# Performance work log

Hardware: AMD Instinct MI355X
Metric: run time of the kernel (lower is better)

The kernel has to match this reference:

```python
import jax, jax.numpy as jnp
import numpy as np

# Swin block config (matches init_kwargs)
NUM_HEADS = 6
WS = 7          # window_size
SHIFT = 3       # shift_size
C = 192         # channels; keras MHA key_dim = channels
KEY_DIM = C


def setup_inputs() -> dict:
    key = jax.random.key(0)
    ks = jax.random.split(key, 9)
    B, H, W = 16, 112, 112
    s = 0.02
    x = jax.random.normal(ks[0], (B, H, W, C), dtype=jnp.float32)
    # keras MultiHeadAttention params: Wq/Wk/Wv [C, heads, key_dim], Wo [heads, key_dim, C]
    Wq = jax.random.normal(ks[1], (C, NUM_HEADS, KEY_DIM), dtype=jnp.float32) * s
    bq = jnp.zeros((NUM_HEADS, KEY_DIM), dtype=jnp.float32)
    Wk = jax.random.normal(ks[2], (C, NUM_HEADS, KEY_DIM), dtype=jnp.float32) * s
    bk = jnp.zeros((NUM_HEADS, KEY_DIM), dtype=jnp.float32)
    Wv = jax.random.normal(ks[3], (C, NUM_HEADS, KEY_DIM), dtype=jnp.float32) * s
    bv = jnp.zeros((NUM_HEADS, KEY_DIM), dtype=jnp.float32)
    Wo = jax.random.normal(ks[4], (NUM_HEADS, KEY_DIM, C), dtype=jnp.float32) * s
    bo = jnp.zeros((C,), dtype=jnp.float32)
    return {"x": x, "Wq": Wq, "bq": bq, "Wk": Wk, "bk": bk,
            "Wv": Wv, "bv": bv, "Wo": Wo, "bo": bo}


def reference(x, Wq, bq, Wk, bk, Wv, bv, Wo, bo):
    B, H, W, _ = x.shape
    # shifted window: roll up-left
    x = jnp.roll(x, shift=(-SHIFT, -SHIFT), axis=(1, 2))
    # window partition (== tf.image.extract_patches + reshape):
    # [B,H,W,C] -> [B*nW, ws*ws, C] with row-major window-token order
    nH, nW = H // WS, W // WS
    win = x.reshape(B, nH, WS, nW, WS, C).transpose(0, 1, 3, 2, 4, 5)
    win = win.reshape(B * nH * nW, WS * WS, C)
    q = jnp.einsum('btc,chd->bthd', win, Wq) + bq
    k = jnp.einsum('btc,chd->bthd', win, Wk) + bk
    v = jnp.einsum('btc,chd->bthd', win, Wv) + bv
    scale = 1.0 / jnp.sqrt(jnp.asarray(KEY_DIM, dtype=q.dtype))
    scores = jnp.einsum('bthd,bshd->bhts', q, k) * scale  # [nWin, heads, 49, 49]
    attn = jax.nn.softmax(scores, axis=-1)
    o = jnp.einsum('bhts,bshd->bthd', attn, v)
    o = jnp.einsum('bthd,hdc->btc', o, Wo) + bo
    # NOTE: original code merges windows with a PLAIN reshape (does not invert
    # the partition); replicate exactly for faithfulness.
    out = o.reshape(B, H, W, C)
    out = jnp.roll(out, shift=(SHIFT, SHIFT), axis=(1, 2))
    return out
```

## Files before the change

kernel.cpp:

```cpp
#include <hip/hip_runtime.h>
#include <hip/hip_bf16.h>

typedef __bf16 bf16_t;
typedef __bf16 bf16x4 __attribute__((ext_vector_type(4)));
typedef __bf16 bf16x8 __attribute__((ext_vector_type(8)));
typedef float  f32x4  __attribute__((ext_vector_type(4)));

#define NH    6
#define CH    192
#define HW    112
#define SHIFT 3

#define XLD 200
#define ULD 72

#define X_OFF   0
#define T_OFF   (64 * XLD)
#define P_OFF   T_OFF
#define VOT_OFF (T_OFF + 64 * ULD)
#define LDS_ELEMS (VOT_OFF + 192 * ULD)
#define LDS_BYTES (LDS_ELEMS * 2)

#define U_OFF_ELEMS  (NH * CH * CH)
#define BU_OFF_BYTES (2 * NH * CH * CH * 2)
#define W1_OFF_BYTES (BU_OFF_BYTES + NH * CH * 4)

__global__ void prep_gt(const float* __restrict__ Wq, const float* __restrict__ Wk,
                        bf16_t* __restrict__ gt) {
  __shared__ float wk_row[CH];
  int h = blockIdx.x / CH, cp = blockIdx.x % CH;
  int c = threadIdx.x;
  wk_row[c] = Wk[(cp * NH + h) * CH + c];
  __syncthreads();
  float acc = 0.f;
  for (int d = 0; d < CH; ++d)
    acc += wk_row[d] * Wq[(c * NH + h) * CH + d];
  int tile = cp >> 4, l15 = cp & 15;
  int ks = c >> 5, lg = (c >> 3) & 3, e = c & 7;
  gt[((((h * 12 + tile) * 6 + ks) << 6) + lg * 16 + l15) * 8 + e] = (bf16_t)acc;
}

__global__ void prep_u(const float* __restrict__ Wv, const float* __restrict__ Wo,
                       bf16_t* __restrict__ u_out) {
  __shared__ float wv_row[CH];
  int h = blockIdx.x / CH, ci = blockIdx.x % CH;
  int t = threadIdx.x;
  wv_row[t] = Wv[(ci * NH + h) * CH + t];
  __syncthreads();
  float acc = 0.f;
  for (int d = 0; d < CH; ++d)
    acc += wv_row[d] * Wo[(h * CH + d) * CH + t];
  int tile = t >> 4, l15 = t & 15;
  int ks = ci >> 5, lg = (ci >> 3) & 3, e = ci & 7;
  u_out[((((h * 12 + tile) * 6 + ks) << 6) + lg * 16 + l15) * 8 + e] = (bf16_t)acc;
}

__global__ void prep_bu(const float* __restrict__ bv, const float* __restrict__ Wo,
                        float* __restrict__ bu) {
  int h = blockIdx.x, c = threadIdx.x;
  float acc = 0.f;
  for (int d = 0; d < CH; ++d)
    acc += bv[h * CH + d] * Wo[(h * CH + d) * CH + c];
  bu[h * CH + c] = acc;
}

__global__ void prep_w1(const float* __restrict__ Wk, const float* __restrict__ bq,
                        float* __restrict__ w1) {
  int h = blockIdx.x, cp = threadIdx.x;
  float acc = 0.f;
  for (int d = 0; d < CH; ++d)
    acc += Wk[(cp * NH + h) * CH + d] * bq[h * CH + d];
  w1[h * CH + cp] = acc;
}

__global__ __launch_bounds__(256, 2) void swin_fused(
    const float* __restrict__ x,
    const float* __restrict__ bo,
    const bf16_t* __restrict__ wts,
    const float* __restrict__ bu, const float* __restrict__ w1,
    float* __restrict__ out) {
  extern __shared__ char smem_raw[];
  bf16_t* lds  = (bf16_t*)smem_raw;
  bf16_t* Xl   = lds + X_OFF;
  bf16_t* Tl   = lds + T_OFF;
  bf16_t* Pl   = lds + P_OFF;
  bf16_t* VOtl = lds + VOT_OFF;

  const int tid  = threadIdx.x;
  const int wave = tid >> 6;
  const int lane = tid & 63;
  const int l15  = lane & 15;
  const int lg   = lane >> 4;

  const int blk = blockIdx.x;
  const int b   = blk >> 8;
  const int rem = blk & 255;
  const int wi  = rem >> 4, wj = rem & 15;

  for (int idx = tid; idx < 15 * 100; idx += 256) {
    int row = 49 + idx / 100, c2 = (idx % 100) * 2;
    *(unsigned int*)&Xl[row * XLD + c2] = 0u;
  }
  for (int idx = tid; idx < 49 * 48; idx += 256) {
    int t = idx / 48, q4 = idx % 48;
    int hs = wi * 7 + t / 7 + SHIFT; if (hs >= HW) hs -= HW;
    int ws2 = wj * 7 + t % 7 + SHIFT; if (ws2 >= HW) ws2 -= HW;
    const float4 v = *(const float4*)&x[(((b * HW + hs) * HW) + ws2) * CH + q4 * 4];
    bf16x4 pk = { (bf16_t)v.x, (bf16_t)v.y, (bf16_t)v.z, (bf16_t)v.w };
    *(bf16x4*)&Xl[t * XLD + q4 * 4] = pk;
  }

  const int wm = wave * 3;
  const float scale = 0.07216878364870322f;
  f32x4 yacc[3][4] = {};

  for (int h = 0; h < NH; ++h) {
    __syncthreads();
    {
      const bf16_t* gt = wts;
      f32x4 acc[3][4] = {};
#pragma unroll
      for (int ks = 0; ks < 6; ++ks) {
        bf16x8 af[3], bfr[4];
#pragma unroll
        for (int mi = 0; mi < 3; ++mi)
          af[mi] = *(const bf16x8*)&gt[((((h * 12 + wm + mi) * 6 + ks) << 6) + lane) * 8];
#pragma unroll
        for (int ni = 0; ni < 4; ++ni)
          bfr[ni] = *(const bf16x8*)&Xl[(ni * 16 + l15) * XLD + ks * 32 + lg * 8];
#pragma unroll
        for (int mi = 0; mi < 3; ++mi)
#pragma unroll
          for (int ni = 0; ni < 4; ++ni)
            acc[mi][ni] = __builtin_amdgcn_mfma_f32_16x16x32_bf16(af[mi], bfr[ni], acc[mi][ni], 0, 0, 0);
      }
      const float* w1h = w1 + h * CH;
#pragma unroll
      for (int mi = 0; mi < 3; ++mi) {
        int cp0 = (wm + mi) * 16 + lg * 4;
        const f32x4 ww = *(const f32x4*)&w1h[cp0];
#pragma unroll
        for (int ni = 0; ni < 4; ++ni) {
          int i = ni * 16 + l15;
          if (i < 49) {
            bf16x4 pk = { (bf16_t)(acc[mi][ni][0] + ww[0]), (bf16_t)(acc[mi][ni][1] + ww[1]),
                          (bf16_t)(acc[mi][ni][2] + ww[2]), (bf16_t)(acc[mi][ni][3] + ww[3]) };
            *(bf16x4*)&Tl[i * XLD + cp0] = pk;
          }
        }
      }
    }
    __syncthreads();
    bf16x4 psave[4];
    f32x4 vacc[3][4] = {};
    const bf16_t* U_w = wts + U_OFF_ELEMS;
    {
      f32x4 sacc[4] = {};
#pragma unroll
      for (int ks = 0; ks < 6; ++ks) {
        bf16x8 af[4], bfu[3];
#pragma unroll
        for (int mi = 0; mi < 4; ++mi)
          af[mi] = *(const bf16x8*)&Xl[(mi * 16 + l15) * XLD + ks * 32 + lg * 8];
        bf16x8 bt = *(const bf16x8*)&Tl[(wave * 16 + l15) * XLD + ks * 32 + lg * 8];
#pragma unroll
        for (int mi = 0; mi < 3; ++mi)
          bfu[mi] = *(const bf16x8*)&U_w[((((h * 12 + wm + mi) * 6 + ks) << 6) + lane) * 8];
#pragma unroll
        for (int mj = 0; mj < 4; ++mj)
          sacc[mj] = __builtin_amdgcn_mfma_f32_16x16x32_bf16(af[mj], bt, sacc[mj], 0, 0, 0);
#pragma unroll
        for (int mi = 0; mi < 3; ++mi)
#pragma unroll
          for (int ms = 0; ms < 4; ++ms)
            vacc[mi][ms] = __builtin_amdgcn_mfma_f32_16x16x32_bf16(af[ms], bfu[mi], vacc[mi][ms], 0, 0, 0);
      }
      float mx = -1e30f;
#pragma unroll
      for (int mj = 0; mj < 4; ++mj)
#pragma unroll
        for (int r = 0; r < 4; ++r) {
          int j = mj * 16 + lg * 4 + r;
          if (j < 49) mx = fmaxf(mx, sacc[mj][r]);
        }
      mx = fmaxf(mx, __shfl_xor(mx, 16));
      mx = fmaxf(mx, __shfl_xor(mx, 32));
      float p[4][4];
      float sum = 0.f;
#pragma unroll
      for (int mj = 0; mj < 4; ++mj)
#pragma unroll
        for (int r = 0; r < 4; ++r) {
          int j = mj * 16 + lg * 4 + r;
          float e = (j < 49) ? __expf((sacc[mj][r] - mx) * scale) : 0.f;
          p[mj][r] = e;
          sum += e;
        }
      sum += __shfl_xor(sum, 16);
      sum += __shfl_xor(sum, 32);
      float inv = 1.f / sum;
#pragma unroll
      for (int mj = 0; mj < 4; ++mj) {
        bf16x4 pk = { (bf16_t)(p[mj][0] * inv), (bf16_t)(p[mj][1] * inv),
                      (bf16_t)(p[mj][2] * inv), (bf16_t)(p[mj][3] * inv) };
        psave[mj] = pk;
      }
    }
    __syncthreads();
    {
      const float* bu_h = bu + h * CH;
      int i = wave * 16 + l15;
#pragma unroll
      for (int mj = 0; mj < 4; ++mj)
        *(bf16x4*)&Pl[i * ULD + mj * 16 + lg * 4] = psave[mj];
#pragma unroll
      for (int mi = 0; mi < 3; ++mi) {
        int c = (wm + mi) * 16 + l15;
        float bb = bu_h[c];
#pragma unroll
        for (int ms = 0; ms < 4; ++ms) {
          int s0 = ms * 16 + lg * 4;
          bf16x4 pk = { (bf16_t)(vacc[mi][ms][0] + bb), (bf16_t)(vacc[mi][ms][1] + bb),
                        (bf16_t)(vacc[mi][ms][2] + bb), (bf16_t)(vacc[mi][ms][3] + bb) };
          *(bf16x4*)&VOtl[c * ULD + s0] = pk;
        }
      }
    }
    __syncthreads();
    {
#pragma unroll
      for (int ks = 0; ks < 2; ++ks) {
        bf16x8 af[3], bfr[4];
#pragma unroll
        for (int mi = 0; mi < 3; ++mi)
          af[mi] = *(const bf16x8*)&VOtl[((wm + mi) * 16 + l15) * ULD + ks * 32 + lg * 8];
#pragma unroll
        for (int ni = 0; ni < 4; ++ni)
          bfr[ni] = *(const bf16x8*)&Pl[(ni * 16 + l15) * ULD + ks * 32 + lg * 8];
#pragma unroll
        for (int mi = 0; mi < 3; ++mi)
#pragma unroll
          for (int ni = 0; ni < 4; ++ni)
            yacc[mi][ni] = __builtin_amdgcn_mfma_f32_16x16x32_bf16(af[mi], bfr[ni], yacc[mi][ni], 0, 0, 0);
      }
    }
  }

#pragma unroll
  for (int ni = 0; ni < 4; ++ni) {
    int t = ni * 16 + l15;
    if (t < 49) {
      int pos = rem * 49 + t;
      int hp = pos / 112, wp = pos % 112;
      hp += SHIFT; if (hp >= HW) hp -= HW;
      wp += SHIFT; if (wp >= HW) wp -= HW;
      float* op = out + (((b * HW + hp) * HW) + wp) * CH;
#pragma unroll
      for (int mi = 0; mi < 3; ++mi) {
        int c0 = (wm + mi) * 16 + lg * 4;
        f32x4 v = yacc[mi][ni];
        v[0] += bo[c0]; v[1] += bo[c0 + 1]; v[2] += bo[c0 + 2]; v[3] += bo[c0 + 3];
        *(f32x4*)&op[c0] = v;
      }
    }
  }
}

extern "C" void kernel_launch(void* const* d_in, const int* in_sizes, int n_in,
                              void* d_out, int out_size, void* d_ws, size_t ws_size,
                              hipStream_t stream) {
  const float* x  = (const float*)d_in[0];
  const float* Wq = (const float*)d_in[1];
  const float* bq = (const float*)d_in[2];
  const float* Wk = (const float*)d_in[3];
  const float* Wv = (const float*)d_in[5];
  const float* bv = (const float*)d_in[6];
  const float* Wo = (const float*)d_in[7];
  const float* bo = (const float*)d_in[8];
  float* out = (float*)d_out;
  bf16_t* wts = (bf16_t*)d_ws;
  float*  bu  = (float*)((char*)d_ws + BU_OFF_BYTES);
  float*  w1  = (float*)((char*)d_ws + W1_OFF_BYTES);

  prep_gt<<<NH * CH, CH, 0, stream>>>(Wq, Wk, wts);
  prep_u<<<NH * CH, CH, 0, stream>>>(Wv, Wo, wts + U_OFF_ELEMS);
  prep_bu<<<NH, CH, 0, stream>>>(bv, Wo, bu);
  prep_w1<<<NH, CH, 0, stream>>>(Wk, bq, w1);

  (void)hipFuncSetAttribute((const void*)swin_fused,
                            hipFuncAttributeMaxDynamicSharedMemorySize, LDS_BYTES);
  swin_fused<<<dim3(4096), dim3(256), LDS_BYTES, stream>>>(x, bo, wts, bu, w1, out);
}
```

Measured before the change: 473.3 us.

## Restructure per-head MFMA loops to cut registers and drop P staging in LDS

Splits the T and VO projections into smaller accumulator chunks and moves the VO computation after softmax, so fewer live accumulators are needed and launch bounds can rise to three blocks per CU. The softmax probabilities stay in registers as MFMA B operands instead of being written to LDS, which removes the P buffer and shrinks the LDS footprint. The output accumulation is re-mapped so each wave owns 16 tokens across all 192 channels. The trade-offs are less operand reuse per LDS/global load, extra unpacking shuffles, and possible register spilling under the tighter bound.

```diff
diff --git a/kernel.cpp b/kernel.cpp
--- a/kernel.cpp
+++ b/kernel.cpp
@@ -16,9 +16,8 @@
 
 #define X_OFF   0
 #define T_OFF   (64 * XLD)
-#define P_OFF   T_OFF
-#define VOT_OFF (T_OFF + 64 * ULD)
-#define LDS_ELEMS (VOT_OFF + 192 * ULD)
+#define VOT_OFF T_OFF
+#define LDS_ELEMS (T_OFF + 192 * ULD)
 #define LDS_BYTES (LDS_ELEMS * 2)
 
 #define U_OFF_ELEMS  (NH * CH * CH)
@@ -73,7 +72,7 @@
   w1[h * CH + cp] = acc;
 }
 
-__global__ __launch_bounds__(256, 2) void swin_fused(
+__global__ __launch_bounds__(256, 3) void swin_fused(
     const float* __restrict__ x,
     const float* __restrict__ bo,
     const bf16_t* __restrict__ wts,
@@ -83,7 +82,6 @@
   bf16_t* lds  = (bf16_t*)smem_raw;
   bf16_t* Xl   = lds + X_OFF;
   bf16_t* Tl   = lds + T_OFF;
-  bf16_t* Pl   = lds + P_OFF;
   bf16_t* VOtl = lds + VOT_OFF;
 
   const int tid  = threadIdx.x;
@@ -112,68 +110,50 @@
 
   const int wm = wave * 3;
   const float scale = 0.07216878364870322f;
-  f32x4 yacc[3][4] = {};
+  f32x4 yacc[12] = {};
 
   for (int h = 0; h < NH; ++h) {
     __syncthreads();
     {
       const bf16_t* gt = wts;
-      f32x4 acc[3][4] = {};
+      const float* w1h = w1 + h * CH;
+#pragma unroll
+      for (int ni = 0; ni < 4; ++ni) {
+        f32x4 acc[3] = {};
+#pragma unroll
+        for (int ks = 0; ks < 6; ++ks) {
+          bf16x8 bfr = *(const bf16x8*)&Xl[(ni * 16 + l15) * XLD + ks * 32 + lg * 8];
+#pragma unroll
+          for (int mi = 0; mi < 3; ++mi) {
+            bf16x8 af = *(const bf16x8*)&gt[((((h * 12 + wm + mi) * 6 + ks) << 6) + lane) * 8];
+            acc[mi] = __builtin_amdgcn_mfma_f32_16x16x32_bf16(af, bfr, acc[mi], 0, 0, 0);
+          }
+        }
+        int i = ni * 16 + l15;
+        if (i < 49) {
+#pragma unroll
+          for (int mi = 0; mi < 3; ++mi) {
+            int cp0 = (wm + mi) * 16 + lg * 4;
+            const f32x4 ww = *(const f32x4*)&w1h[cp0];
+            bf16x4 pk = { (bf16_t)(acc[mi][0] + ww[0]), (bf16_t)(acc[mi][1] + ww[1]),
+                          (bf16_t)(acc[mi][2] + ww[2]), (bf16_t)(acc[mi][3] + ww[3]) };
+            *(bf16x4*)&Tl[i * XLD + cp0] = pk;
+          }
+        }
+      }
+    }
+    __syncthreads();
+    bf16x4 psave[4];
+    {
+      f32x4 sacc[4] = {};
 #pragma unroll
       for (int ks = 0; ks < 6; ++ks) {
-        bf16x8 af[3], bfr[4];
-#pragma unroll
-        for (int mi = 0; mi < 3; ++mi)
-          af[mi] = *(const bf16x8*)&gt[((((h * 12 + wm + mi) * 6 + ks) << 6) + lane) * 8];
-#pragma unroll
-        for (int ni = 0; ni < 4; ++ni)
-          bfr[ni] = *(const bf16x8*)&Xl[(ni * 16 + l15) * XLD + ks * 32 + lg * 8];
-#pragma unroll
-        for (int mi = 0; mi < 3; ++mi)
-#pragma unroll
-          for (int ni = 0; ni < 4; ++ni)
-            acc[mi][ni] = __builtin_amdgcn_mfma_f32_16x16x32_bf16(af[mi], bfr[ni], acc[mi][ni], 0, 0, 0);
-      }
-      const float* w1h = w1 + h * CH;
-#pragma unroll
-      for (int mi = 0; mi < 3; ++mi) {
-        int cp0 = (wm + mi) * 16 + lg * 4;
-        const f32x4 ww = *(const f32x4*)&w1h[cp0];
-#pragma unroll
-        for (int ni = 0; ni < 4; ++ni) {
-          int i = ni * 16 + l15;
-          if (i < 49) {
-            bf16x4 pk = { (bf16_t)(acc[mi][ni][0] + ww[0]), (bf16_t)(acc[mi][ni][1] + ww[1]),
-                          (bf16_t)(acc[mi][ni][2] + ww[2]), (bf16_t)(acc[mi][ni][3] + ww[3]) };
-            *(bf16x4*)&Tl[i * XLD + cp0] = pk;
-          }
-        }
-      }
-    }
-    __syncthreads();
-    bf16x4 psave[4];
-    f32x4 vacc[3][4] = {};
-    const bf16_t* U_w = wts + U_OFF_ELEMS;
-    {
-      f32x4 sacc[4] = {};
-#pragma unroll
-      for (int ks = 0; ks < 6; ++ks) {
-        bf16x8 af[4], bfu[3];
-#pragma unroll
-        for (int mi = 0; mi < 4; ++mi)
-          af[mi] = *(const bf16x8*)&Xl[(mi * 16 + l15) * XLD + ks * 32 + lg * 8];
         bf16x8 bt = *(const bf16x8*)&Tl[(wave * 16 + l15) * XLD + ks * 32 + lg * 8];
 #pragma unroll
-        for (int mi = 0; mi < 3; ++mi)
-          bfu[mi] = *(const bf16x8*)&U_w[((((h * 12 + wm + mi) * 6 + ks) << 6) + lane) * 8];
-#pragma unroll
-        for (int mj = 0; mj < 4; ++mj)
-          sacc[mj] = __builtin_amdgcn_mfma_f32_16x16x32_bf16(af[mj], bt, sacc[mj], 0, 0, 0);
-#pragma unroll
-        for (int mi = 0; mi < 3; ++mi)
-#pragma unroll
-          for (int ms = 0; ms < 4; ++ms)
-            vacc[mi][ms] = __builtin_amdgcn_mfma_f32_16x16x32_bf16(af[ms], bfu[mi], vacc[mi][ms], 0, 0, 0);
+        for (int mj = 0; mj < 4; ++mj) {
+          bf16x8 af = *(const bf16x8*)&Xl[(mj * 16 + l15) * XLD + ks * 32 + lg * 8];
+          sacc[mj] = __builtin_amdgcn_mfma_f32_16x16x32_bf16(af, bt, sacc[mj], 0, 0, 0);
+        }
       }
       float mx = -1e30f;
 #pragma unroll
@@ -208,47 +188,55 @@
     }
     __syncthreads();
     {
+      const bf16_t* U_w = wts + U_OFF_ELEMS;
       const float* bu_h = bu + h * CH;
-      int i = wave * 16 + l15;
-#pragma unroll
-      for (int mj = 0; mj < 4; ++mj)
-        *(bf16x4*)&Pl[i * ULD + mj * 16 + lg * 4] = psave[mj];
 #pragma unroll
       for (int mi = 0; mi < 3; ++mi) {
         int c = (wm + mi) * 16 + l15;
         float bb = bu_h[c];
 #pragma unroll
-        for (int ms = 0; ms < 4; ++ms) {
-          int s0 = ms * 16 + lg * 4;
-          bf16x4 pk = { (bf16_t)(vacc[mi][ms][0] + bb), (bf16_t)(vacc[mi][ms][1] + bb),
-                        (bf16_t)(vacc[mi][ms][2] + bb), (bf16_t)(vacc[mi][ms][3] + bb) };
-          *(bf16x4*)&VOtl[c * ULD + s0] = pk;
-        }
-      }
-    }
-    __syncthreads();
-    {
-#pragma unroll
-      for (int ks = 0; ks < 2; ++ks) {
-        bf16x8 af[3], bfr[4];
-#pragma unroll
-        for (int mi = 0; mi < 3; ++mi)
-          af[mi] = *(const bf16x8*)&VOtl[((wm + mi) * 16 + l15) * ULD + ks * 32 + lg * 8];
-#pragma unroll
-        for (int ni = 0; ni < 4; ++ni)
-          bfr[ni] = *(const bf16x8*)&Pl[(ni * 16 + l15) * ULD + ks * 32 + lg * 8];
-#pragma unroll
-        for (int mi = 0; mi < 3; ++mi)
-#pragma unroll
-          for (int ni = 0; ni < 4; ++ni)
-            yacc[mi][ni] = __builtin_amdgcn_mfma_f32_16x16x32_bf16(af[mi], bfr[ni], yacc[mi][ni], 0, 0, 0);
-      }
-    }
-  }
-
-#pragma unroll
-  for (int ni = 0; ni < 4; ++ni) {
-    int t = ni * 16 + l15;
+        for (int sh = 0; sh < 2; ++sh) {
+          f32x4 vacc[2] = {};
+#pragma unroll
+          for (int ks = 0; ks < 6; ++ks) {
+            bf16x8 bfu = *(const bf16x8*)&U_w[((((h * 12 + wm + mi) * 6 + ks) << 6) + lane) * 8];
+#pragma unroll
+            for (int m2 = 0; m2 < 2; ++m2) {
+              bf16x8 af = *(const bf16x8*)&Xl[((sh * 2 + m2) * 16 + l15) * XLD + ks * 32 + lg * 8];
+              vacc[m2] = __builtin_amdgcn_mfma_f32_16x16x32_bf16(af, bfu, vacc[m2], 0, 0, 0);
+            }
+          }
+#pragma unroll
+          for (int m2 = 0; m2 < 2; ++m2) {
+            int s0 = (sh * 2 + m2) * 16 + lg * 4;
+            bf16x4 pk = { (bf16_t)(vacc[m2][0] + bb), (bf16_t)(vacc[m2][1] + bb),
+                          (bf16_t)(vacc[m2][2] + bb), (bf16_t)(vacc[m2][3] + bb) };
+            *(bf16x4*)&VOtl[c * ULD + s0] = pk;
+          }
+        }
+      }
+    }
+    __syncthreads();
+    {
+      bf16x8 bq8[2];
+      bq8[0] = __builtin_shufflevector(psave[0], psave[1], 0, 1, 2, 3, 4, 5, 6, 7);
+      bq8[1] = __builtin_shufflevector(psave[2], psave[3], 0, 1, 2, 3, 4, 5, 6, 7);
+#pragma unroll
+      for (int mc = 0; mc < 12; ++mc) {
+#pragma unroll
+        for (int kp = 0; kp < 2; ++kp) {
+          const bf16_t* vr = &VOtl[(mc * 16 + l15) * ULD + kp * 32 + lg * 4];
+          bf16x4 a0 = *(const bf16x4*)vr;
+          bf16x4 a1 = *(const bf16x4*)(vr + 16);
+          bf16x8 av = __builtin_shufflevector(a0, a1, 0, 1, 2, 3, 4, 5, 6, 7);
+          yacc[mc] = __builtin_amdgcn_mfma_f32_16x16x32_bf16(av, bq8[kp], yacc[mc], 0, 0, 0);
+        }
+      }
+    }
+  }
+
+  {
+    int t = wave * 16 + l15;
     if (t < 49) {
       int pos = rem * 49 + t;
       int hp = pos / 112, wp = pos % 112;
@@ -256,9 +244,9 @@
       wp += SHIFT; if (wp >= HW) wp -= HW;
       float* op = out + (((b * HW + hp) * HW) + wp) * CH;
 #pragma unroll
-      for (int mi = 0; mi < 3; ++mi) {
-        int c0 = (wm + mi) * 16 + lg * 4;
-        f32x4 v = yacc[mi][ni];
+      for (int mc = 0; mc < 12; ++mc) {
+        int c0 = mc * 16 + lg * 4;
+        f32x4 v = yacc[mc];
         v[0] += bo[c0]; v[1] += bo[c0 + 1]; v[2] += bo[c0 + 2]; v[3] += bo[c0 + 3];
         *(f32x4*)&op[c0] = v;
       }
```

Result: slower. 861.0 us (+81.9%).

## Keep softmax probabilities in registers and defer the PV product to the next head

Applied to the files above, without the earlier changes.

Each wave now keeps its own query rows' softmax probabilities in registers as MFMA B-operands instead of writing them to a shared P buffer. The P·V product is remapped so each wave accumulates all 192 output channels for its 16 tokens. That product is software-pipelined one head behind, running alongside the next head's score computation. This removes the P LDS round trip and one barrier per head, and the V projection is moved after the softmax. In exchange it adds register pressure (12 accumulators plus carried P fragments) and split LDS reads of V.

```diff
diff --git a/kernel.cpp b/kernel.cpp
--- a/kernel.cpp
+++ b/kernel.cpp
@@ -16,8 +16,7 @@
 
 #define X_OFF   0
 #define T_OFF   (64 * XLD)
-#define P_OFF   T_OFF
-#define VOT_OFF (T_OFF + 64 * ULD)
+#define VOT_OFF (2 * 64 * XLD)
 #define LDS_ELEMS (VOT_OFF + 192 * ULD)
 #define LDS_BYTES (LDS_ELEMS * 2)
 
@@ -83,7 +82,6 @@
   bf16_t* lds  = (bf16_t*)smem_raw;
   bf16_t* Xl   = lds + X_OFF;
   bf16_t* Tl   = lds + T_OFF;
-  bf16_t* Pl   = lds + P_OFF;
   bf16_t* VOtl = lds + VOT_OFF;
 
   const int tid  = threadIdx.x;
@@ -109,13 +107,14 @@
     bf16x4 pk = { (bf16_t)v.x, (bf16_t)v.y, (bf16_t)v.z, (bf16_t)v.w };
     *(bf16x4*)&Xl[t * XLD + q4 * 4] = pk;
   }
+  __syncthreads();
 
   const int wm = wave * 3;
   const float scale = 0.07216878364870322f;
-  f32x4 yacc[3][4] = {};
+  f32x4 yacc[12] = {};
+  bf16x8 pq_prev0 = {}, pq_prev1 = {};
 
   for (int h = 0; h < NH; ++h) {
-    __syncthreads();
     {
       const bf16_t* gt = wts;
       f32x4 acc[3][4] = {};
@@ -151,29 +150,35 @@
       }
     }
     __syncthreads();
-    bf16x4 psave[4];
-    f32x4 vacc[3][4] = {};
-    const bf16_t* U_w = wts + U_OFF_ELEMS;
     {
       f32x4 sacc[4] = {};
 #pragma unroll
       for (int ks = 0; ks < 6; ++ks) {
-        bf16x8 af[4], bfu[3];
-#pragma unroll
-        for (int mi = 0; mi < 4; ++mi)
-          af[mi] = *(const bf16x8*)&Xl[(mi * 16 + l15) * XLD + ks * 32 + lg * 8];
         bf16x8 bt = *(const bf16x8*)&Tl[(wave * 16 + l15) * XLD + ks * 32 + lg * 8];
 #pragma unroll
-        for (int mi = 0; mi < 3; ++mi)
-          bfu[mi] = *(const bf16x8*)&U_w[((((h * 12 + wm + mi) * 6 + ks) << 6) + lane) * 8];
-#pragma unroll
-        for (int mj = 0; mj < 4; ++mj)
-          sacc[mj] = __builtin_amdgcn_mfma_f32_16x16x32_bf16(af[mj], bt, sacc[mj], 0, 0, 0);
-#pragma unroll
-        for (int mi = 0; mi < 3; ++mi)
-#pragma unroll
-          for (int ms = 0; ms < 4; ++ms)
-            vacc[mi][ms] = __builtin_amdgcn_mfma_f32_16x16x32_bf16(af[ms], bfu[mi], vacc[mi][ms], 0, 0, 0);
+        for (int mj = 0; mj < 4; ++mj) {
+          bf16x8 af = *(const bf16x8*)&Xl[(mj * 16 + l15) * XLD + ks * 32 + lg * 8];
+          sacc[mj] = __builtin_amdgcn_mfma_f32_16x16x32_bf16(af, bt, sacc[mj], 0, 0, 0);
+        }
+      }
+      if (h > 0) {
+#pragma unroll
+        for (int mc = 0; mc < 12; ++mc) {
+          {
+            const bf16_t* vr = &VOtl[(mc * 16 + l15) * ULD + 0 * 32 + lg * 4];
+            bf16x4 a0 = *(const bf16x4*)vr;
+            bf16x4 a1 = *(const bf16x4*)(vr + 16);
+            bf16x8 av = __builtin_shufflevector(a0, a1, 0, 1, 2, 3, 4, 5, 6, 7);
+            yacc[mc] = __builtin_amdgcn_mfma_f32_16x16x32_bf16(av, pq_prev0, yacc[mc], 0, 0, 0);
+          }
+          {
+            const bf16_t* vr = &VOtl[(mc * 16 + l15) * ULD + 1 * 32 + lg * 4];
+            bf16x4 a0 = *(const bf16x4*)vr;
+            bf16x4 a1 = *(const bf16x4*)(vr + 16);
+            bf16x8 av = __builtin_shufflevector(a0, a1, 0, 1, 2, 3, 4, 5, 6, 7);
+            yacc[mc] = __builtin_amdgcn_mfma_f32_16x16x32_bf16(av, pq_prev1, yacc[mc], 0, 0, 0);
+          }
+        }
       }
       float mx = -1e30f;
 #pragma unroll
@@ -199,20 +204,37 @@
       sum += __shfl_xor(sum, 16);
       sum += __shfl_xor(sum, 32);
       float inv = 1.f / sum;
-#pragma unroll
-      for (int mj = 0; mj < 4; ++mj) {
-        bf16x4 pk = { (bf16_t)(p[mj][0] * inv), (bf16_t)(p[mj][1] * inv),
-                      (bf16_t)(p[mj][2] * inv), (bf16_t)(p[mj][3] * inv) };
-        psave[mj] = pk;
-      }
+      bf16x4 ps0 = { (bf16_t)(p[0][0] * inv), (bf16_t)(p[0][1] * inv),
+                     (bf16_t)(p[0][2] * inv), (bf16_t)(p[0][3] * inv) };
+      bf16x4 ps1 = { (bf16_t)(p[1][0] * inv), (bf16_t)(p[1][1] * inv),
+                     (bf16_t)(p[1][2] * inv), (bf16_t)(p[1][3] * inv) };
+      bf16x4 ps2 = { (bf16_t)(p[2][0] * inv), (bf16_t)(p[2][1] * inv),
+                     (bf16_t)(p[2][2] * inv), (bf16_t)(p[2][3] * inv) };
+      bf16x4 ps3 = { (bf16_t)(p[3][0] * inv), (bf16_t)(p[3][1] * inv),
+                     (bf16_t)(p[3][2] * inv), (bf16_t)(p[3][3] * inv) };
+      pq_prev0 = __builtin_shufflevector(ps0, ps1, 0, 1, 2, 3, 4, 5, 6, 7);
+      pq_prev1 = __builtin_shufflevector(ps2, ps3, 0, 1, 2, 3, 4, 5, 6, 7);
     }
     __syncthreads();
     {
+      const bf16_t* U_w = wts + U_OFF_ELEMS;
       const float* bu_h = bu + h * CH;
-      int i = wave * 16 + l15;
-#pragma unroll
-      for (int mj = 0; mj < 4; ++mj)
-        *(bf16x4*)&Pl[i * ULD + mj * 16 + lg * 4] = psave[mj];
+      f32x4 vacc[3][4] = {};
+#pragma unroll
+      for (int ks = 0; ks < 6; ++ks) {
+        bf16x8 bfu[3], af[4];
+#pragma unroll
+        for (int mi = 0; mi < 3; ++mi)
+          bfu[mi] = *(const bf16x8*)&U_w[((((h * 12 + wm + mi) * 6 + ks) << 6) + lane) * 8];
+#pragma unroll
+        for (int ms = 0; ms < 4; ++ms)
+          af[ms] = *(const bf16x8*)&Xl[(ms * 16 + l15) * XLD + ks * 32 + lg * 8];
+#pragma unroll
+        for (int mi = 0; mi < 3; ++mi)
+#pragma unroll
+          for (int ms = 0; ms < 4; ++ms)
+            vacc[mi][ms] = __builtin_amdgcn_mfma_f32_16x16x32_bf16(af[ms], bfu[mi], vacc[mi][ms], 0, 0, 0);
+      }
 #pragma unroll
       for (int mi = 0; mi < 3; ++mi) {
         int c = (wm + mi) * 16 + l15;
@@ -227,28 +249,30 @@
       }
     }
     __syncthreads();
-    {
-#pragma unroll
-      for (int ks = 0; ks < 2; ++ks) {
-        bf16x8 af[3], bfr[4];
-#pragma unroll
-        for (int mi = 0; mi < 3; ++mi)
-          af[mi] = *(const bf16x8*)&VOtl[((wm + mi) * 16 + l15) * ULD + ks * 32 + lg * 8];
-#pragma unroll
-        for (int ni = 0; ni < 4; ++ni)
-          bfr[ni] = *(const bf16x8*)&Pl[(ni * 16 + l15) * ULD + ks * 32 + lg * 8];
-#pragma unroll
-        for (int mi = 0; mi < 3; ++mi)
-#pragma unroll
-          for (int ni = 0; ni < 4; ++ni)
-            yacc[mi][ni] = __builtin_amdgcn_mfma_f32_16x16x32_bf16(af[mi], bfr[ni], yacc[mi][ni], 0, 0, 0);
-      }
-    }
-  }
-
-#pragma unroll
-  for (int ni = 0; ni < 4; ++ni) {
-    int t = ni * 16 + l15;
+  }
+
+  {
+#pragma unroll
+    for (int mc = 0; mc < 12; ++mc) {
+      {
+        const bf16_t* vr = &VOtl[(mc * 16 + l15) * ULD + 0 * 32 + lg * 4];
+        bf16x4 a0 = *(const bf16x4*)vr;
+        bf16x4 a1 = *(const bf16x4*)(vr + 16);
+        bf16x8 av = __builtin_shufflevector(a0, a1, 0, 1, 2, 3, 4, 5, 6, 7);
+        yacc[mc] = __builtin_amdgcn_mfma_f32_16x16x32_bf16(av, pq_prev0, yacc[mc], 0, 0, 0);
+      }
+      {
+        const bf16_t* vr = &VOtl[(mc * 16 + l15) * ULD + 1 * 32 + lg * 4];
+        bf16x4 a0 = *(const bf16x4*)vr;
+        bf16x4 a1 = *(const bf16x4*)(vr + 16);
+        bf16x8 av = __builtin_shufflevector(a0, a1, 0, 1, 2, 3, 4, 5, 6, 7);
+        yacc[mc] = __builtin_amdgcn_mfma_f32_16x16x32_bf16(av, pq_prev1, yacc[mc], 0, 0, 0);
+      }
+    }
+  }
+
+  {
+    int t = wave * 16 + l15;
     if (t < 49) {
       int pos = rem * 49 + t;
       int hp = pos / 112, wp = pos % 112;
@@ -256,9 +280,9 @@
       wp += SHIFT; if (wp >= HW) wp -= HW;
       float* op = out + (((b * HW + hp) * HW) + wp) * CH;
 #pragma unroll
-      for (int mi = 0; mi < 3; ++mi) {
-        int c0 = (wm + mi) * 16 + lg * 4;
-        f32x4 v = yacc[mi][ni];
+      for (int mc = 0; mc < 12; ++mc) {
+        int c0 = mc * 16 + lg * 4;
+        f32x4 v = yacc[mc];
         v[0] += bo[c0]; v[1] += bo[c0 + 1]; v[2] += bo[c0 + 2]; v[3] += bo[c0 + 3];
         *(f32x4*)&op[c0] = v;
       }
```

Measured after the change: 475.5 us. About the same (+0.5%).

## Double-buffer T/P across heads and keep V·Wo fragments in registers

Applied to the files above, without the earlier changes.

Restructures the per-head loop. The T projection for head h+1 is computed into an alternate LDS buffer while head h's P is consumed, which cuts barriers per head from four to one. The VU product is now produced directly in the MFMA operand layout and kept in registers instead of being staged through LDS, and the output GEMM swaps operand roles, which changes the final store pattern to scalar per-lane writes. Risks are higher register pressure, padding rows of X left uninitialized (their results are masked only partly), and less coalesced output stores.

```diff
diff --git a/kernel.cpp b/kernel.cpp
--- a/kernel.cpp
+++ b/kernel.cpp
@@ -12,13 +12,14 @@
 #define SHIFT 3
 
 #define XLD 200
-#define ULD 72
+#define PLD 68
 
 #define X_OFF   0
-#define T_OFF   (64 * XLD)
-#define P_OFF   T_OFF
-#define VOT_OFF (T_OFF + 64 * ULD)
-#define LDS_ELEMS (VOT_OFF + 192 * ULD)
+#define T0_OFF  9800
+#define T1_OFF  19600
+#define P0_OFF  29400
+#define P1_OFF  33752
+#define LDS_ELEMS 38104
 #define LDS_BYTES (LDS_ELEMS * 2)
 
 #define U_OFF_ELEMS  (NH * CH * CH)
@@ -73,6 +74,52 @@
   w1[h * CH + cp] = acc;
 }
 
+__device__ __forceinline__ void t_phase(const bf16_t* __restrict__ gt,
+                                        const float* __restrict__ w1h,
+                                        const bf16_t* Xl, bf16_t* Tdst,
+                                        int hh, int wm, int lane, int l15, int lg) {
+  f32x4 ww[3];
+#pragma unroll
+  for (int mi = 0; mi < 3; ++mi)
+    ww[mi] = *(const f32x4*)&w1h[(wm + mi) * 16 + lg * 4];
+#pragma unroll
+  for (int ip = 0; ip < 2; ++ip) {
+    f32x4 acc[3][2];
+#pragma unroll
+    for (int mi = 0; mi < 3; ++mi)
+#pragma unroll
+      for (int n2 = 0; n2 < 2; ++n2) acc[mi][n2] = ww[mi];
+#pragma unroll
+    for (int ks = 0; ks < 6; ++ks) {
+      bf16x8 af[3], bfr[2];
+#pragma unroll
+      for (int mi = 0; mi < 3; ++mi)
+        af[mi] = *(const bf16x8*)&gt[((((hh * 12 + wm + mi) * 6 + ks) << 6) + lane) * 8];
+#pragma unroll
+      for (int n2 = 0; n2 < 2; ++n2)
+        bfr[n2] = *(const bf16x8*)&Xl[((ip * 2 + n2) * 16 + l15) * XLD + ks * 32 + lg * 8];
+#pragma unroll
+      for (int mi = 0; mi < 3; ++mi)
+#pragma unroll
+        for (int n2 = 0; n2 < 2; ++n2)
+          acc[mi][n2] = __builtin_amdgcn_mfma_f32_16x16x32_bf16(af[mi], bfr[n2], acc[mi][n2], 0, 0, 0);
+    }
+#pragma unroll
+    for (int mi = 0; mi < 3; ++mi) {
+      int cp0 = (wm + mi) * 16 + lg * 4;
+#pragma unroll
+      for (int n2 = 0; n2 < 2; ++n2) {
+        int i = (ip * 2 + n2) * 16 + l15;
+        if (i < 49) {
+          bf16x4 pk = { (bf16_t)acc[mi][n2][0], (bf16_t)acc[mi][n2][1],
+                        (bf16_t)acc[mi][n2][2], (bf16_t)acc[mi][n2][3] };
+          *(bf16x4*)&Tdst[i * XLD + cp0] = pk;
+        }
+      }
+    }
+  }
+}
+
 __global__ __launch_bounds__(256, 2) void swin_fused(
     const float* __restrict__ x,
     const float* __restrict__ bo,
@@ -80,11 +127,8 @@
     const float* __restrict__ bu, const float* __restrict__ w1,
     float* __restrict__ out) {
   extern __shared__ char smem_raw[];
-  bf16_t* lds  = (bf16_t*)smem_raw;
-  bf16_t* Xl   = lds + X_OFF;
-  bf16_t* Tl   = lds + T_OFF;
-  bf16_t* Pl   = lds + P_OFF;
-  bf16_t* VOtl = lds + VOT_OFF;
+  bf16_t* lds = (bf16_t*)smem_raw;
+  bf16_t* Xl  = lds + X_OFF;
 
   const int tid  = threadIdx.x;
   const int wave = tid >> 6;
@@ -97,10 +141,6 @@
   const int rem = blk & 255;
   const int wi  = rem >> 4, wj = rem & 15;
 
-  for (int idx = tid; idx < 15 * 100; idx += 256) {
-    int row = 49 + idx / 100, c2 = (idx % 100) * 2;
-    *(unsigned int*)&Xl[row * XLD + c2] = 0u;
-  }
   for (int idx = tid; idx < 49 * 48; idx += 256) {
     int t = idx / 48, q4 = idx % 48;
     int hs = wi * 7 + t / 7 + SHIFT; if (hs >= HW) hs -= HW;
@@ -109,71 +149,31 @@
     bf16x4 pk = { (bf16_t)v.x, (bf16_t)v.y, (bf16_t)v.z, (bf16_t)v.w };
     *(bf16x4*)&Xl[t * XLD + q4 * 4] = pk;
   }
+  __syncthreads();
 
   const int wm = wave * 3;
   const float scale = 0.07216878364870322f;
+
+  t_phase(wts, w1, Xl, lds + T0_OFF, 0, wm, lane, l15, lg);
+  __syncthreads();
+
   f32x4 yacc[3][4] = {};
 
   for (int h = 0; h < NH; ++h) {
-    __syncthreads();
-    {
-      const bf16_t* gt = wts;
-      f32x4 acc[3][4] = {};
-#pragma unroll
-      for (int ks = 0; ks < 6; ++ks) {
-        bf16x8 af[3], bfr[4];
-#pragma unroll
-        for (int mi = 0; mi < 3; ++mi)
-          af[mi] = *(const bf16x8*)&gt[((((h * 12 + wm + mi) * 6 + ks) << 6) + lane) * 8];
-#pragma unroll
-        for (int ni = 0; ni < 4; ++ni)
-          bfr[ni] = *(const bf16x8*)&Xl[(ni * 16 + l15) * XLD + ks * 32 + lg * 8];
-#pragma unroll
-        for (int mi = 0; mi < 3; ++mi)
-#pragma unroll
-          for (int ni = 0; ni < 4; ++ni)
-            acc[mi][ni] = __builtin_amdgcn_mfma_f32_16x16x32_bf16(af[mi], bfr[ni], acc[mi][ni], 0, 0, 0);
-      }
-      const float* w1h = w1 + h * CH;
-#pragma unroll
-      for (int mi = 0; mi < 3; ++mi) {
-        int cp0 = (wm + mi) * 16 + lg * 4;
-        const f32x4 ww = *(const f32x4*)&w1h[cp0];
-#pragma unroll
-        for (int ni = 0; ni < 4; ++ni) {
-          int i = ni * 16 + l15;
-          if (i < 49) {
-            bf16x4 pk = { (bf16_t)(acc[mi][ni][0] + ww[0]), (bf16_t)(acc[mi][ni][1] + ww[1]),
-                          (bf16_t)(acc[mi][ni][2] + ww[2]), (bf16_t)(acc[mi][ni][3] + ww[3]) };
-            *(bf16x4*)&Tl[i * XLD + cp0] = pk;
-          }
-        }
-      }
-    }
-    __syncthreads();
+    const bf16_t* Tcur = lds + ((h & 1) ? T1_OFF : T0_OFF);
+    bf16_t*       Pcur = lds + ((h & 1) ? P1_OFF : P0_OFF);
+
     bf16x4 psave[4];
-    f32x4 vacc[3][4] = {};
-    const bf16_t* U_w = wts + U_OFF_ELEMS;
     {
       f32x4 sacc[4] = {};
 #pragma unroll
       for (int ks = 0; ks < 6; ++ks) {
-        bf16x8 af[4], bfu[3];
-#pragma unroll
-        for (int mi = 0; mi < 4; ++mi)
-          af[mi] = *(const bf16x8*)&Xl[(mi * 16 + l15) * XLD + ks * 32 + lg * 8];
-        bf16x8 bt = *(const bf16x8*)&Tl[(wave * 16 + l15) * XLD + ks * 32 + lg * 8];
-#pragma unroll
-        for (int mi = 0; mi < 3; ++mi)
-          bfu[mi] = *(const bf16x8*)&U_w[((((h * 12 + wm + mi) * 6 + ks) << 6) + lane) * 8];
-#pragma unroll
-        for (int mj = 0; mj < 4; ++mj)
-          sacc[mj] = __builtin_amdgcn_mfma_f32_16x16x32_bf16(af[mj], bt, sacc[mj], 0, 0, 0);
-#pragma unroll
-        for (int mi = 0; mi < 3; ++mi)
-#pragma unroll
-          for (int ms = 0; ms < 4; ++ms)
-            vacc[mi][ms] = __builtin_amdgcn_mfma_f32_16x16x32_bf16(af[ms], bfu[mi], vacc[mi][ms], 0, 0, 0);
+        bf16x8 bt = *(const bf16x8*)&Tcur[(wave * 16 + l15) * XLD + ks * 32 + lg * 8];
+#pragma unroll
+        for (int mj = 0; mj < 4; ++mj) {
+          bf16x8 af = *(const bf16x8*)&Xl[(mj * 16 + l15) * XLD + ks * 32 + lg * 8];
+          sacc[mj] = __builtin_amdgcn_mfma_f32_16x16x32_bf16(af, bt, sacc[mj], 0, 0, 0);
+        }
       }
       float mx = -1e30f;
 #pragma unroll
@@ -206,61 +206,83 @@
         psave[mj] = pk;
       }
     }
+    {
+      int irow = wave * 16 + l15;
+#pragma unroll
+      for (int mj = 0; mj < 4; ++mj)
+        *(bf16x4*)&Pcur[irow * PLD + mj * 16 + lg * 4] = psave[mj];
+    }
+    if (h + 1 < NH)
+      t_phase(wts, w1 + (h + 1) * CH, Xl, lds + (((h + 1) & 1) ? T1_OFF : T0_OFF),
+              h + 1, wm, lane, l15, lg);
+    bf16x8 bfrag[3][2];
+    {
+      const bf16_t* U_w = wts + U_OFF_ELEMS;
+      const float* bu_h = bu + h * CH;
+#pragma unroll
+      for (int mi = 0; mi < 3; ++mi) {
+        const f32x4 bbv = *(const f32x4*)&bu_h[(wm + mi) * 16 + lg * 4];
+        f32x4 vacc[4];
+#pragma unroll
+        for (int ms = 0; ms < 4; ++ms) vacc[ms] = bbv;
+#pragma unroll
+        for (int ks = 0; ks < 6; ++ks) {
+          bf16x8 bfu = *(const bf16x8*)&U_w[((((h * 12 + wm + mi) * 6 + ks) << 6) + lane) * 8];
+#pragma unroll
+          for (int ms = 0; ms < 4; ++ms) {
+            bf16x8 af = *(const bf16x8*)&Xl[(ms * 16 + l15) * XLD + ks * 32 + lg * 8];
+            vacc[ms] = __builtin_amdgcn_mfma_f32_16x16x32_bf16(af, bfu, vacc[ms], 0, 0, 0);
+          }
+        }
+        if (lg) { vacc[3] = (f32x4){0.f, 0.f, 0.f, 0.f}; }
+        else    { vacc[3][1] = 0.f; vacc[3][2] = 0.f; vacc[3][3] = 0.f; }
+#pragma unroll
+        for (int kp = 0; kp < 2; ++kp) {
+          bf16x4 lo = { (bf16_t)vacc[2 * kp][0], (bf16_t)vacc[2 * kp][1],
+                        (bf16_t)vacc[2 * kp][2], (bf16_t)vacc[2 * kp][3] };
+          bf16x4 hi = { (bf16_t)vacc[2 * kp + 1][0], (bf16_t)vacc[2 * kp + 1][1],
+                        (bf16_t)vacc[2 * kp + 1][2], (bf16_t)vacc[2 * kp + 1][3] };
+          bfrag[mi][kp] = __builtin_shufflevector(lo, hi, 0, 1, 2, 3, 4, 5, 6, 7);
+        }
+      }
+    }
     __syncthreads();
     {
-      const float* bu_h = bu + h * CH;
-      int i = wave * 16 + l15;
-#pragma unroll
-      for (int mj = 0; mj < 4; ++mj)
-        *(bf16x4*)&Pl[i * ULD + mj * 16 + lg * 4] = psave[mj];
-#pragma unroll
-      for (int mi = 0; mi < 3; ++mi) {
-        int c = (wm + mi) * 16 + l15;
-        float bb = bu_h[c];
-#pragma unroll
-        for (int ms = 0; ms < 4; ++ms) {
-          int s0 = ms * 16 + lg * 4;
-          bf16x4 pk = { (bf16_t)(vacc[mi][ms][0] + bb), (bf16_t)(vacc[mi][ms][1] + bb),
-                        (bf16_t)(vacc[mi][ms][2] + bb), (bf16_t)(vacc[mi][ms][3] + bb) };
-          *(bf16x4*)&VOtl[c * ULD + s0] = pk;
-        }
-      }
-    }
-    __syncthreads();
-    {
-#pragma unroll
-      for (int ks = 0; ks < 2; ++ks) {
-        bf16x8 af[3], bfr[4];
-#pragma unroll
-        for (int mi = 0; mi < 3; ++mi)
-          af[mi] = *(const bf16x8*)&VOtl[((wm + mi) * 16 + l15) * ULD + ks * 32 + lg * 8];
-#pragma unroll
-        for (int ni = 0; ni < 4; ++ni)
-          bfr[ni] = *(const bf16x8*)&Pl[(ni * 16 + l15) * ULD + ks * 32 + lg * 8];
-#pragma unroll
-        for (int mi = 0; mi < 3; ++mi)
-#pragma unroll
-          for (int ni = 0; ni < 4; ++ni)
-            yacc[mi][ni] = __builtin_amdgcn_mfma_f32_16x16x32_bf16(af[mi], bfr[ni], yacc[mi][ni], 0, 0, 0);
+#pragma unroll
+      for (int ni = 0; ni < 4; ++ni) {
+#pragma unroll
+        for (int kp = 0; kp < 2; ++kp) {
+          const bf16_t* pr = &Pcur[(ni * 16 + l15) * PLD + kp * 32 + lg * 4];
+          bf16x4 a0 = *(const bf16x4*)pr;
+          bf16x4 a1 = *(const bf16x4*)(pr + 16);
+          bf16x8 af8 = __builtin_shufflevector(a0, a1, 0, 1, 2, 3, 4, 5, 6, 7);
+#pragma unroll
+          for (int mi = 0; mi < 3; ++mi)
+            yacc[mi][ni] = __builtin_amdgcn_mfma_f32_16x16x32_bf16(af8, bfrag[mi][kp], yacc[mi][ni], 0, 0, 0);
+        }
       }
     }
   }
 
-#pragma unroll
-  for (int ni = 0; ni < 4; ++ni) {
-    int t = ni * 16 + l15;
-    if (t < 49) {
-      int pos = rem * 49 + t;
-      int hp = pos / 112, wp = pos % 112;
-      hp += SHIFT; if (hp >= HW) hp -= HW;
-      wp += SHIFT; if (wp >= HW) wp -= HW;
-      float* op = out + (((b * HW + hp) * HW) + wp) * CH;
-#pragma unroll
-      for (int mi = 0; mi < 3; ++mi) {
-        int c0 = (wm + mi) * 16 + lg * 4;
-        f32x4 v = yacc[mi][ni];
-        v[0] += bo[c0]; v[1] += bo[c0 + 1]; v[2] += bo[c0 + 2]; v[3] += bo[c0 + 3];
-        *(f32x4*)&op[c0] = v;
+  {
+    float bov[3];
+#pragma unroll
+    for (int mi = 0; mi < 3; ++mi) bov[mi] = bo[(wm + mi) * 16 + l15];
+#pragma unroll
+    for (int ni = 0; ni < 4; ++ni) {
+#pragma unroll
+      for (int r = 0; r < 4; ++r) {
+        int t = ni * 16 + lg * 4 + r;
+        if (t < 49) {
+          int pos = rem * 49 + t;
+          int hp = pos / 112, wp = pos % 112;
+          hp += SHIFT; if (hp >= HW) hp -= HW;
+          wp += SHIFT; if (wp >= HW) wp -= HW;
+          float* op = out + (((b * HW + hp) * HW) + wp) * CH + l15;
+#pragma unroll
+          for (int mi = 0; mi < 3; ++mi)
+            op[(wm + mi) * 16] = yacc[mi][ni][r] + bov[mi];
+        }
       }
     }
   }
```

After: 409.6 us. 1.16x faster.
